# Kernel tuning notes

Hardware: AMD Instinct MI355X
Metric: run time of the kernel (lower is better)

The kernel has to match this reference:

```python
import jax, jax.numpy as jnp
import numpy as np

B, S, H, NH = 4, 2048, 1024, 16
D = H // NH  # head width = 64
SCALE = 1.0 / np.sqrt(np.float32(H))  # NOTE: module scales by rsqrt(hidden_size), not head_width
EPS = 1e-5


def setup_inputs() -> dict:
    key = jax.random.key(0)
    ks = jax.random.split(key, 12)
    def lin(k):
        kw, kb = jax.random.split(k)
        return (jax.random.normal(kw, (H, H), jnp.float32) * 0.02,
                jax.random.normal(kb, (H,), jnp.float32) * 0.02)
    Wq, bq = lin(ks[0]); Wk, bk = lin(ks[1]); Wv, bv = lin(ks[2]); Wm, bm = lin(ks[3])
    q = jax.random.normal(ks[4], (B, S, H), jnp.float32)
    k = jax.random.normal(ks[5], (B, S, H), jnp.float32)
    v = jax.random.normal(ks[6], (B, S, H), jnp.float32)
    # causal mask: True positions are masked with -inf (matches masked_fill semantics)
    mask = jnp.broadcast_to(jnp.triu(jnp.ones((S, S), bool), k=1), (B, S, S))
    gamma = jnp.ones((H,), jnp.float32)
    beta = jnp.zeros((H,), jnp.float32)
    return {"q": q, "k": k, "v": v, "mask": mask,
            "Wq": Wq, "bq": bq, "Wk": Wk, "bk": bk, "Wv": Wv, "bv": bv,
            "Wm": Wm, "bm": bm, "gamma": gamma, "beta": beta}


def layer_norm(x, gamma, beta):
    mu = jnp.mean(x, axis=-1, keepdims=True)
    var = jnp.mean(jnp.square(x - mu), axis=-1, keepdims=True)
    return (x - mu) * jax.lax.rsqrt(var + EPS) * gamma + beta


def reference(q, k, v, mask, Wq, bq, Wk, bk, Wv, bv, Wm, bm, gamma, beta):
    residual = q
    # projections, split into heads: [B, NH, S, D]
    qh = (q @ Wq.T + bq).reshape(B, S, NH, D).transpose(0, 2, 1, 3)
    kh = (k @ Wk.T + bk).reshape(B, S, NH, D).transpose(0, 2, 1, 3)
    vh = (v @ Wv.T + bv).reshape(B, S, NH, D).transpose(0, 2, 1, 3)
    scores = jnp.einsum('bhsd,bhtd->bhst', qh, kh) * SCALE
    scores = jnp.where(mask[:, None, :, :], -jnp.inf, scores)
    attn = jax.nn.softmax(scores, axis=-1)  # dropout is identity (p=0 / eval)
    ctx = jnp.einsum('bhst,bhtd->bhsd', attn, vh)
    ctx = ctx.transpose(0, 2, 1, 3).reshape(B, S, H)
    out = ctx @ Wm.T + bm
    out = layer_norm(out + residual, gamma, beta)
    return out, attn
```

## Files before the change

### kernel.cpp

```cpp
#include <hip/hip_runtime.h>
#include <hip/hip_bf16.h>

#define S_LEN   2048
#define NHEAD   16
#define HID     1024
#define HDIM    64
#define ATT_SCALE 0.03125f
#define LN_EPS  1e-5f
#define EXP_C1  0.04508422002778011f
#define EXP_C2  (-11.541560327111707f)

using bf16x8 = __attribute__((ext_vector_type(8))) short;
using f32x4  = __attribute__((ext_vector_type(4))) float;
using u16x8  = __attribute__((ext_vector_type(8))) unsigned short;
typedef unsigned short u16;

__device__ __forceinline__ u16 f2b(float f) {
  union { float f; unsigned u; } v; v.f = f;
  unsigned r = v.u + 0x7fffu + ((v.u >> 16) & 1u);
  return (u16)(r >> 16);
}

__device__ __forceinline__ float fexp2(float x) {
  return __builtin_amdgcn_exp2f(x);
}

__device__ __forceinline__ unsigned cvtpk(float a, float b) {
  unsigned r;
  asm("v_cvt_pk_bf16_f32 %0, %1, %2" : "=v"(r) : "v"(a), "v"(b));
  return r;
}

__device__ __forceinline__ f32x4 mfma16(bf16x8 a, bf16x8 b, f32x4 c) {
  return __builtin_amdgcn_mfma_f32_16x16x32_bf16(a, b, c, 0, 0, 0);
}

__device__ __forceinline__ void gld_lds16(const u16* g, void* l) {
  __builtin_amdgcn_global_load_lds(
      (const __attribute__((address_space(1))) void*)g,
      (__attribute__((address_space(3))) void*)l, 16, 0, 0);
}

__global__ void cvt_f32_bf16(const float* __restrict__ src, u16* __restrict__ dst, int n4) {
  int i = blockIdx.x * blockDim.x + threadIdx.x;
  int stride = gridDim.x * blockDim.x;
  for (; i < n4; i += stride) {
    float4 v = ((const float4*)src)[i];
    ushort4 o;
    o.x = f2b(v.x); o.y = f2b(v.y); o.z = f2b(v.z); o.w = f2b(v.w);
    ((ushort4*)dst)[i] = o;
  }
}

template<int EPI>
__global__ __launch_bounds__(256) void gemm_bt(
    const u16* __restrict__ A, const u16* __restrict__ W,
    const float* __restrict__ bias, u16* __restrict__ out_b,
    float* __restrict__ out_f, int M, int N, int K,
    float* __restrict__ fill, int fphase)
{
  __shared__ __align__(16) u16 As[128 * 64];
  __shared__ __align__(16) u16 Bs[128 * 64];
  const int t = threadIdx.x;

  if (blockIdx.y >= 64) {
    int u = (((int)blockIdx.y - 64) * 8 + (int)blockIdx.x) * 3 + fphase;
    if (u < 7680) {
      int bh = u & 63, tmp = u >> 6, qtb = tmp >> 3, rg = tmp & 7;
      int w4 = (15 - qtb) * 32;
      f32x4* base = (f32x4*)(fill + ((long)bh * 2048 + qtb * 128 + rg * 16) * 2048
                                  + (qtb + 1) * 128);
      f32x4 z = { 0.f, 0.f, 0.f, 0.f };
      for (int r = 0; r < 16; ++r) {
        f32x4* rp = base + (long)r * 512;
        for (int cc = t; cc < w4; cc += 256) rp[cc] = z;
      }
    }
    return;
  }

  const int m0 = blockIdx.y * 128, n0 = blockIdx.x * 128;
  const int w = t >> 6, lane = t & 63, g = lane >> 4, c = lane & 15;
  const int wr = w >> 1, wc = w & 1;

  f32x4 acc[4][4] = {};

  for (int k0 = 0; k0 < K; k0 += 64) {
    __syncthreads();
#pragma unroll
    for (int it = 0; it < 4; ++it) {
      int chunk = it * 256 + t;
      int row = chunk >> 3, cf = (chunk & 7) * 8;
      gld_lds16(&A[(long)(m0 + row) * K + k0 + cf], &As[(it * 256 + (t & ~63)) * 8]);
      gld_lds16(&W[(long)(n0 + row) * K + k0 + cf], &Bs[(it * 256 + (t & ~63)) * 8]);
    }
    __syncthreads();
#pragma unroll
    for (int kk = 0; kk < 2; ++kk) {
      bf16x8 am[4], bn[4];
#pragma unroll
      for (int m = 0; m < 4; ++m)
        am[m] = *(const bf16x8*)(&As[(wr * 64 + m * 16 + c) * 64 + kk * 32 + g * 8]);
#pragma unroll
      for (int n = 0; n < 4; ++n)
        bn[n] = *(const bf16x8*)(&Bs[(wc * 64 + n * 16 + c) * 64 + kk * 32 + g * 8]);
#pragma unroll
      for (int m = 0; m < 4; ++m)
#pragma unroll
        for (int n = 0; n < 4; ++n)
          acc[m][n] = mfma16(am[m], bn[n], acc[m][n]);
    }
  }

#pragma unroll
  for (int m = 0; m < 4; ++m)
#pragma unroll
    for (int n = 0; n < 4; ++n)
#pragma unroll
      for (int r = 0; r < 4; ++r) {
        int grow = m0 + wr * 64 + m * 16 + g * 4 + r;
        int gcol = n0 + wc * 64 + n * 16 + c;
        float v = acc[m][n][r];
        if (EPI == 0) {
          v += bias[gcol];
          int b = grow >> 11, s = grow & 2047;
          int h = gcol >> 6, d = gcol & 63;
          out_b[(((long)(b * 16 + h) * 2048 + s) << 6) + d] = f2b(v);
        } else {
          out_f[(long)grow * N + gcol] = v;
        }
      }
}

__global__ __launch_bounds__(256) void transpose_v(const u16* __restrict__ vh,
                                                   u16* __restrict__ vt) {
  __shared__ __align__(16) u16 tile[64 * 72];
  const int t = threadIdx.x;
  const u16* src = vh + ((long)blockIdx.y * 2048 + blockIdx.x * 64) * 64;
#pragma unroll
  for (int it = 0; it < 2; ++it) {
    int chunk = it * 256 + t;
    int s = chunk >> 3, d0 = (chunk & 7) * 8;
    *(int4*)(&tile[s * 72 + d0]) = *(const int4*)(&src[s * 64 + d0]);
  }
  __syncthreads();
  u16* dst = vt + (long)blockIdx.y * 64 * 2048 + blockIdx.x * 64;
#pragma unroll
  for (int it = 0; it < 2; ++it) {
    int chunk = it * 256 + t;
    int d = chunk >> 3, s0 = (chunk & 7) * 8;
    u16x8 v;
#pragma unroll
    for (int x = 0; x < 8; ++x) v[x] = tile[(s0 + x) * 72 + d];
    *(u16x8*)(&dst[(long)d * 2048 + s0]) = v;
  }
}

__global__ __launch_bounds__(512, 4) void attn_kernel(
    const u16* __restrict__ qh, const u16* __restrict__ kh,
    const u16* __restrict__ vt, u16* __restrict__ ctx,
    float* __restrict__ attn)
{
  __shared__ __align__(16) char lds[81920];
  const int t = threadIdx.x, w = t >> 6, lane = t & 63, g = lane >> 4, c = lane & 15;
  const int n = blockIdx.x;
  const int bh = (n & 7) * 8 + ((n >> 3) & 7);
  const int qtb = 15 - (n >> 6);
  const int q0 = qtb * 128;
  const int ktmax = qtb * 2 + 1;
  const long kvbase = (long)bh * 2048 * 64;

  bf16x8 qa[2];
  {
    const u16* qp = qh + kvbase + (long)(q0 + w * 16 + c) * 64 + g * 8;
    qa[0] = *(const bf16x8*)(qp);
    qa[1] = *(const bf16x8*)(qp + 32);
  }
  const int qpos = q0 + w * 16 + c;

  const int srow = t >> 3, sc8 = t & 7;
  const int ksoff = srow * 64 + ((sc8 ^ (srow & 7)) * 8);
  const u16* kbase = kh + kvbase;
  const u16* vbase = vt + (long)(bh * 64 + srow) * 2048 + ((sc8 ^ (srow & 7)) * 8);

  float lsum = 0.f;
  {
    gld_lds16(kbase + ksoff, lds + w * 1024);
    gld_lds16(kbase + 4096 + ksoff, lds + 8192 + w * 1024);
    for (int p = 0; p <= qtb; ++p) {
      const int kb = (p & 1) * 16384;
      if (p < qtb) {
        const int nb = ((p + 1) & 1) * 16384;
        gld_lds16(kbase + (long)(p + 1) * 8192 + ksoff, lds + nb + w * 1024);
        gld_lds16(kbase + (long)(p + 1) * 8192 + 4096 + ksoff, lds + nb + 8192 + w * 1024);
        asm volatile("s_waitcnt vmcnt(2)" ::: "memory");
      } else {
        asm volatile("s_waitcnt vmcnt(0)" ::: "memory");
      }
      __builtin_amdgcn_sched_barrier(0);
      __builtin_amdgcn_s_barrier();
      __builtin_amdgcn_sched_barrier(0);
      f32x4 sacc[8] = {};
      __builtin_amdgcn_s_setprio(1);
#pragma unroll
      for (int sub = 0; sub < 8; ++sub) {
        int row = sub * 16 + c;
#pragma unroll
        for (int kk = 0; kk < 2; ++kk) {
          bf16x8 av = *(const bf16x8*)(lds + kb + row * 128 + (((kk * 4 + g) ^ (c & 7)) << 4));
          sacc[sub] = mfma16(av, qa[kk], sacc[sub]);
        }
      }
      __builtin_amdgcn_s_setprio(0);
#pragma unroll
      for (int sub = 0; sub < 8; ++sub)
#pragma unroll
        for (int r = 0; r < 4; ++r) {
          int kpos = p * 128 + sub * 16 + g * 4 + r;
          float e = fexp2(fmaf(sacc[sub][r], EXP_C1, EXP_C2));
          lsum += (kpos > qpos) ? 0.f : e;
        }
      __builtin_amdgcn_sched_barrier(0);
      __builtin_amdgcn_s_barrier();
    }
  }
  lsum += __shfl_xor(lsum, 16, 64);
  lsum += __shfl_xor(lsum, 32, 64);
  const float ri = 1.f / lsum;

  char* const Ps = lds + 32768 + w * 2048;
  char* const Pf = lds + 49152 + w * 4096;
  f32x4 oacc[4] = {};
  gld_lds16(kbase + ksoff, lds + w * 1024);
  gld_lds16(vbase, lds + 16384 + w * 1024);
  for (int kt = 0; kt <= ktmax; ++kt) {
    const int kb = (kt & 1) * 8192;
    if (kt < ktmax) {
      const int nb = ((kt + 1) & 1) * 8192;
      gld_lds16(kbase + (long)(kt + 1) * 4096 + ksoff, lds + nb + w * 1024);
      gld_lds16(vbase + (kt + 1) * 64, lds + 16384 + nb + w * 1024);
      if (kt == 0) { asm volatile("s_waitcnt vmcnt(2)" ::: "memory"); }
      else         { asm volatile("s_waitcnt vmcnt(6)" ::: "memory"); }
    } else {
      asm volatile("s_waitcnt vmcnt(4)" ::: "memory");
    }
    __builtin_amdgcn_sched_barrier(0);
    __builtin_amdgcn_s_barrier();
    __builtin_amdgcn_sched_barrier(0);
    f32x4 sacc[4] = {};
    __builtin_amdgcn_s_setprio(1);
#pragma unroll
    for (int sub = 0; sub < 4; ++sub) {
      int row = sub * 16 + c;
#pragma unroll
      for (int kk = 0; kk < 2; ++kk) {
        bf16x8 av = *(const bf16x8*)(lds + kb + row * 128 + (((kk * 4 + g) ^ (c & 7)) << 4));
        sacc[sub] = mfma16(av, qa[kk], sacc[sub]);
      }
    }
    __builtin_amdgcn_s_setprio(0);
#pragma unroll
    for (int sub = 0; sub < 4; ++sub) {
      float p[4];
#pragma unroll
      for (int r = 0; r < 4; ++r) {
        int kpos = kt * 64 + sub * 16 + g * 4 + r;
        float e = fexp2(fmaf(sacc[sub][r], EXP_C1, EXP_C2)) * ri;
        p[r] = (kpos > qpos) ? 0.f : e;
      }
      f32x4 pv4 = { p[0], p[1], p[2], p[3] };
      int kgrp = sub * 4 + g;
      *(f32x4*)(Pf + c * 256 + ((kgrp ^ c) & 15) * 16) = pv4;
      uint2 pk = { cvtpk(p[0], p[1]), cvtpk(p[2], p[3]) };
      int chunk = sub * 2 + (g >> 1);
      *(uint2*)(Ps + c * 128 + ((chunk ^ (c & 7)) << 4) + (g & 1) * 8) = pk;
    }
    {
      float* arow0 = attn + ((long)bh * 2048 + q0 + w * 16) * 2048 + kt * 64;
#pragma unroll
      for (int j = 0; j < 4; ++j) {
        int row = j * 4 + g;
        f32x4 pv = *(const f32x4*)(Pf + row * 256 + ((c ^ row) & 15) * 16);
        *(f32x4*)(arow0 + (long)row * 2048 + c * 4) = pv;
      }
    }
    __builtin_amdgcn_s_setprio(1);
#pragma unroll
    for (int kk = 0; kk < 2; ++kk) {
      bf16x8 pa = *(const bf16x8*)(Ps + c * 128 + (((kk * 4 + g) ^ (c & 7)) << 4));
#pragma unroll
      for (int db = 0; db < 4; ++db) {
        bf16x8 vb = *(const bf16x8*)(lds + 16384 + kb + (db * 16 + c) * 128 + (((kk * 4 + g) ^ (c & 7)) << 4));
        oacc[db] = mfma16(pa, vb, oacc[db]);
      }
    }
    __builtin_amdgcn_s_setprio(0);
    __builtin_amdgcn_sched_barrier(0);
    __builtin_amdgcn_s_barrier();
  }

  {
    int b = bh >> 4, h = bh & 15;
#pragma unroll
    for (int db = 0; db < 4; ++db)
#pragma unroll
      for (int r = 0; r < 4; ++r) {
        int s = q0 + w * 16 + g * 4 + r;
        ctx[(long)(b * 2048 + s) * 1024 + h * 64 + db * 16 + c] = f2b(oacc[db][r]);
      }
  }
}

__global__ __launch_bounds__(256) void ln_kernel(
    const float* __restrict__ y, const float* __restrict__ bm,
    const float* __restrict__ resid, const float* __restrict__ gamma,
    const float* __restrict__ beta, float* __restrict__ out)
{
  __shared__ float red[8];
  const long row = blockIdx.x;
  const int t = threadIdx.x, w = t >> 6, lane = t & 63;
  const float4* yp = (const float4*)(y + row * 1024);
  const float4* rp = (const float4*)(resid + row * 1024);
  float4 x = yp[t], rv = rp[t], bv = ((const float4*)bm)[t];
  x.x += rv.x + bv.x; x.y += rv.y + bv.y; x.z += rv.z + bv.z; x.w += rv.w + bv.w;

  float s1 = x.x + x.y + x.z + x.w;
#pragma unroll
  for (int o = 32; o; o >>= 1) s1 += __shfl_xor(s1, o, 64);
  if (!lane) red[w] = s1;
  __syncthreads();
  float mean = (red[0] + red[1] + red[2] + red[3]) * (1.f / 1024.f);

  float dx = x.x - mean, dy = x.y - mean, dz = x.z - mean, dw = x.w - mean;
  float s2 = dx * dx + dy * dy + dz * dz + dw * dw;
#pragma unroll
  for (int o = 32; o; o >>= 1) s2 += __shfl_xor(s2, o, 64);
  if (!lane) red[4 + w] = s2;
  __syncthreads();
  float var = (red[4] + red[5] + red[6] + red[7]) * (1.f / 1024.f);
  float rs = rsqrtf(var + LN_EPS);

  float4 gv = ((const float4*)gamma)[t], be = ((const float4*)beta)[t];
  float4 o4;
  o4.x = dx * rs * gv.x + be.x;
  o4.y = dy * rs * gv.y + be.y;
  o4.z = dz * rs * gv.z + be.z;
  o4.w = dw * rs * gv.w + be.w;
  ((float4*)(out + row * 1024))[t] = o4;
}

extern "C" void kernel_launch(void* const* d_in, const int* in_sizes, int n_in,
                              void* d_out, int out_size, void* d_ws, size_t ws_size,
                              hipStream_t stream) {
  const float* q     = (const float*)d_in[0];
  const float* k     = (const float*)d_in[1];
  const float* v     = (const float*)d_in[2];
  const float* Wq    = (const float*)d_in[4];
  const float* bq    = (const float*)d_in[5];
  const float* Wk    = (const float*)d_in[6];
  const float* bk    = (const float*)d_in[7];
  const float* Wv    = (const float*)d_in[8];
  const float* bv    = (const float*)d_in[9];
  const float* Wm    = (const float*)d_in[10];
  const float* bm    = (const float*)d_in[11];
  const float* gamma = (const float*)d_in[12];
  const float* beta  = (const float*)d_in[13];

  float* out  = (float*)d_out;
  float* attn = out + 8388608;

  char* ws = (char*)d_ws;
  u16* qh   = (u16*)(ws);
  u16* kh   = (u16*)(ws + 16777216);
  u16* vt   = (u16*)(ws + 33554432);
  u16* ctx  = (u16*)(ws + 50331648);
  u16* Wqb  = (u16*)(ws + 67108864);
  u16* Wkb  = Wqb + 1048576;
  u16* Wvb  = Wkb + 1048576;
  u16* Wmb  = Wvb + 1048576;
  u16* xb   = (u16*)(ws + 75497472);
  u16* vh   = (u16*)(ws + 92274688);
  float* y  = (float*)(ws + 75497472);

  const int M = 8192, N = 1024, K = 1024;
  dim3 blk(256);
  dim3 ggrid(8, 64);
  dim3 ggridF(8, 64 + 320);

  cvt_f32_bf16<<<512, blk, 0, stream>>>(Wq, Wqb, 262144);
  cvt_f32_bf16<<<512, blk, 0, stream>>>(Wk, Wkb, 262144);
  cvt_f32_bf16<<<512, blk, 0, stream>>>(Wv, Wvb, 262144);
  cvt_f32_bf16<<<512, blk, 0, stream>>>(Wm, Wmb, 262144);

  cvt_f32_bf16<<<2048, blk, 0, stream>>>(q, xb, 2097152);
  gemm_bt<0><<<ggridF, blk, 0, stream>>>(xb, Wqb, bq, qh, nullptr, M, N, K, attn, 0);
  cvt_f32_bf16<<<2048, blk, 0, stream>>>(k, xb, 2097152);
  gemm_bt<0><<<ggridF, blk, 0, stream>>>(xb, Wkb, bk, kh, nullptr, M, N, K, attn, 1);
  cvt_f32_bf16<<<2048, blk, 0, stream>>>(v, xb, 2097152);
  gemm_bt<0><<<ggridF, blk, 0, stream>>>(xb, Wvb, bv, vh, nullptr, M, N, K, attn, 2);

  transpose_v<<<dim3(32, 64), blk, 0, stream>>>(vh, vt);

  attn_kernel<<<1024, 512, 0, stream>>>(qh, kh, vt, ctx, attn);

  gemm_bt<1><<<ggrid, blk, 0, stream>>>(ctx, Wmb, nullptr, nullptr, y, M, N, K, nullptr, 0);

  ln_kernel<<<8192, blk, 0, stream>>>(y, bm, q, gamma, beta, out);
}
```

Before: 508.1 us.

## Fuse input fp32-to-bf16 conversion into a single batched QKV projection GEMM

Merges the four weight conversions into one launch and replaces three separate convert-plus-GEMM pairs with a single QKV GEMM kernel. That kernel loads fp32 activations directly, packs them to bf16 in registers and stores them into LDS, with the causal-mask zero fill interleaved as extra blocks. This removes the intermediate bf16 activation buffer round-trip and several kernel launches. The cost is that A-tile loads now go through registers instead of async global-to-LDS copies and read twice the bytes. The vh workspace now aliases ctx.

```diff
diff --git a/kernel.cpp b/kernel.cpp
--- a/kernel.cpp
+++ b/kernel.cpp
@@ -12,7 +12,6 @@
 
 using bf16x8 = __attribute__((ext_vector_type(8))) short;
 using f32x4  = __attribute__((ext_vector_type(4))) float;
-using u16x8  = __attribute__((ext_vector_type(8))) unsigned short;
 typedef unsigned short u16;
 
 __device__ __forceinline__ u16 f2b(float f) {
@@ -41,58 +40,134 @@
       (__attribute__((address_space(3))) void*)l, 16, 0, 0);
 }
 
-__global__ void cvt_f32_bf16(const float* __restrict__ src, u16* __restrict__ dst, int n4) {
-  int i = blockIdx.x * blockDim.x + threadIdx.x;
-  int stride = gridDim.x * blockDim.x;
-  for (; i < n4; i += stride) {
-    float4 v = ((const float4*)src)[i];
+__global__ __launch_bounds__(256) void cvt_w4(
+    const float* __restrict__ s0, const float* __restrict__ s1,
+    const float* __restrict__ s2, const float* __restrict__ s3,
+    u16* __restrict__ d0, u16* __restrict__ d1,
+    u16* __restrict__ d2, u16* __restrict__ d3)
+{
+  int i = blockIdx.x * 256 + threadIdx.x;
+  int stride = gridDim.x * 256;
+  for (; i < 1048576; i += stride) {
+    int seg = i >> 18, off = i & 262143;
+    const float* s = seg == 0 ? s0 : seg == 1 ? s1 : seg == 2 ? s2 : s3;
+    u16*         d = seg == 0 ? d0 : seg == 1 ? d1 : seg == 2 ? d2 : d3;
+    float4 vv = ((const float4*)s)[off];
     ushort4 o;
-    o.x = f2b(v.x); o.y = f2b(v.y); o.z = f2b(v.z); o.w = f2b(v.w);
-    ((ushort4*)dst)[i] = o;
-  }
-}
-
-template<int EPI>
-__global__ __launch_bounds__(256) void gemm_bt(
+    o.x = f2b(vv.x); o.y = f2b(vv.y); o.z = f2b(vv.z); o.w = f2b(vv.w);
+    ((ushort4*)d)[off] = o;
+  }
+}
+
+__global__ __launch_bounds__(256) void qkv_gemm(
+    const float* __restrict__ qx, const float* __restrict__ kx,
+    const float* __restrict__ vx,
+    const u16* __restrict__ Wq, const u16* __restrict__ Wk,
+    const u16* __restrict__ Wv,
+    const float* __restrict__ bq, const float* __restrict__ bk,
+    const float* __restrict__ bv,
+    u16* __restrict__ qo, u16* __restrict__ ko, u16* __restrict__ vo,
+    float* __restrict__ fill)
+{
+  const int t = threadIdx.x;
+  const int yg = blockIdx.y / 6, yr = blockIdx.y % 6;
+
+  if (yr != 0) {
+    int u = (yg * 5 + (yr - 1)) * 8 + blockIdx.x;
+    int bh = u & 63, tmp = u >> 6, qtb = tmp >> 3, rg = tmp & 7;
+    int w4 = (15 - qtb) * 32;
+    f32x4* base = (f32x4*)(fill + ((long)bh * 2048 + qtb * 128 + rg * 16) * 2048
+                                + (qtb + 1) * 128);
+    f32x4 z = { 0.f, 0.f, 0.f, 0.f };
+    for (int r = 0; r < 16; ++r) {
+      f32x4* rp = base + (long)r * 512;
+      for (int cc = t; cc < w4; cc += 256) rp[cc] = z;
+    }
+    return;
+  }
+
+  const int op = yg >> 6;
+  const float* A32  = op == 0 ? qx : op == 1 ? kx : vx;
+  const u16*   W    = op == 0 ? Wq : op == 1 ? Wk : Wv;
+  const float* bias = op == 0 ? bq : op == 1 ? bk : bv;
+  u16*         out  = op == 0 ? qo : op == 1 ? ko : vo;
+
+  __shared__ __align__(16) u16 As[128 * 64];
+  __shared__ __align__(16) u16 Bs[128 * 64];
+  const int m0 = (yg & 63) * 128, n0 = blockIdx.x * 128;
+  const int w = t >> 6, lane = t & 63, g = lane >> 4, c = lane & 15;
+  const int wr = w >> 1, wc = w & 1;
+
+  f32x4 acc[4][4] = {};
+
+  for (int k0 = 0; k0 < 1024; k0 += 64) {
+    __syncthreads();
+#pragma unroll
+    for (int it = 0; it < 4; ++it) {
+      int chunk = it * 256 + t;
+      int row = chunk >> 3, cf = (chunk & 7) * 8;
+      const float* ap = &A32[(long)(m0 + row) * 1024 + k0 + cf];
+      float4 a0 = *(const float4*)(ap);
+      float4 a1 = *(const float4*)(ap + 4);
+      uint4 pk = { cvtpk(a0.x, a0.y), cvtpk(a0.z, a0.w),
+                   cvtpk(a1.x, a1.y), cvtpk(a1.z, a1.w) };
+      *(uint4*)(&As[chunk * 8]) = pk;
+      gld_lds16(&W[(long)(n0 + row) * 1024 + k0 + cf], &Bs[(it * 256 + (t & ~63)) * 8]);
+    }
+    __syncthreads();
+#pragma unroll
+    for (int kk = 0; kk < 2; ++kk) {
+      bf16x8 am[4], bn[4];
+#pragma unroll
+      for (int m = 0; m < 4; ++m)
+        am[m] = *(const bf16x8*)(&As[(wr * 64 + m * 16 + c) * 64 + kk * 32 + g * 8]);
+#pragma unroll
+      for (int n = 0; n < 4; ++n)
+        bn[n] = *(const bf16x8*)(&Bs[(wc * 64 + n * 16 + c) * 64 + kk * 32 + g * 8]);
+#pragma unroll
+      for (int m = 0; m < 4; ++m)
+#pragma unroll
+        for (int n = 0; n < 4; ++n)
+          acc[m][n] = mfma16(am[m], bn[n], acc[m][n]);
+    }
+  }
+
+#pragma unroll
+  for (int m = 0; m < 4; ++m)
+#pragma unroll
+    for (int n = 0; n < 4; ++n)
+#pragma unroll
+      for (int r = 0; r < 4; ++r) {
+        int grow = m0 + wr * 64 + m * 16 + g * 4 + r;
+        int gcol = n0 + wc * 64 + n * 16 + c;
+        float v = acc[m][n][r] + bias[gcol];
+        int b = grow >> 11, s = grow & 2047;
+        int h = gcol >> 6, d = gcol & 63;
+        out[(((long)(b * 16 + h) * 2048 + s) << 6) + d] = f2b(v);
+      }
+}
+
+__global__ __launch_bounds__(256) void gemm_out(
     const u16* __restrict__ A, const u16* __restrict__ W,
-    const float* __restrict__ bias, u16* __restrict__ out_b,
-    float* __restrict__ out_f, int M, int N, int K,
-    float* __restrict__ fill, int fphase)
+    float* __restrict__ out_f)
 {
   __shared__ __align__(16) u16 As[128 * 64];
   __shared__ __align__(16) u16 Bs[128 * 64];
   const int t = threadIdx.x;
-
-  if (blockIdx.y >= 64) {
-    int u = (((int)blockIdx.y - 64) * 8 + (int)blockIdx.x) * 3 + fphase;
-    if (u < 7680) {
-      int bh = u & 63, tmp = u >> 6, qtb = tmp >> 3, rg = tmp & 7;
-      int w4 = (15 - qtb) * 32;
-      f32x4* base = (f32x4*)(fill + ((long)bh * 2048 + qtb * 128 + rg * 16) * 2048
-                                  + (qtb + 1) * 128);
-      f32x4 z = { 0.f, 0.f, 0.f, 0.f };
-      for (int r = 0; r < 16; ++r) {
-        f32x4* rp = base + (long)r * 512;
-        for (int cc = t; cc < w4; cc += 256) rp[cc] = z;
-      }
-    }
-    return;
-  }
-
   const int m0 = blockIdx.y * 128, n0 = blockIdx.x * 128;
   const int w = t >> 6, lane = t & 63, g = lane >> 4, c = lane & 15;
   const int wr = w >> 1, wc = w & 1;
 
   f32x4 acc[4][4] = {};
 
-  for (int k0 = 0; k0 < K; k0 += 64) {
+  for (int k0 = 0; k0 < 1024; k0 += 64) {
     __syncthreads();
 #pragma unroll
     for (int it = 0; it < 4; ++it) {
       int chunk = it * 256 + t;
       int row = chunk >> 3, cf = (chunk & 7) * 8;
-      gld_lds16(&A[(long)(m0 + row) * K + k0 + cf], &As[(it * 256 + (t & ~63)) * 8]);
-      gld_lds16(&W[(long)(n0 + row) * K + k0 + cf], &Bs[(it * 256 + (t & ~63)) * 8]);
+      gld_lds16(&A[(long)(m0 + row) * 1024 + k0 + cf], &As[(it * 256 + (t & ~63)) * 8]);
+      gld_lds16(&W[(long)(n0 + row) * 1024 + k0 + cf], &Bs[(it * 256 + (t & ~63)) * 8]);
     }
     __syncthreads();
 #pragma unroll
@@ -120,15 +195,7 @@
       for (int r = 0; r < 4; ++r) {
         int grow = m0 + wr * 64 + m * 16 + g * 4 + r;
         int gcol = n0 + wc * 64 + n * 16 + c;
-        float v = acc[m][n][r];
-        if (EPI == 0) {
-          v += bias[gcol];
-          int b = grow >> 11, s = grow & 2047;
-          int h = gcol >> 6, d = gcol & 63;
-          out_b[(((long)(b * 16 + h) * 2048 + s) << 6) + d] = f2b(v);
-        } else {
-          out_f[(long)grow * N + gcol] = v;
-        }
+        out_f[(long)grow * 1024 + gcol] = acc[m][n][r];
       }
 }
 
@@ -149,10 +216,10 @@
   for (int it = 0; it < 2; ++it) {
     int chunk = it * 256 + t;
     int d = chunk >> 3, s0 = (chunk & 7) * 8;
-    u16x8 v;
+    __attribute__((ext_vector_type(8))) unsigned short v;
 #pragma unroll
     for (int x = 0; x < 8; ++x) v[x] = tile[(s0 + x) * 72 + d];
-    *(u16x8*)(&dst[(long)d * 2048 + s0]) = v;
+    *(decltype(v)*)(&dst[(long)d * 2048 + s0]) = v;
   }
 }
 
@@ -373,37 +440,26 @@
   u16* qh   = (u16*)(ws);
   u16* kh   = (u16*)(ws + 16777216);
   u16* vt   = (u16*)(ws + 33554432);
+  u16* vh   = (u16*)(ws + 50331648);
   u16* ctx  = (u16*)(ws + 50331648);
   u16* Wqb  = (u16*)(ws + 67108864);
   u16* Wkb  = Wqb + 1048576;
   u16* Wvb  = Wkb + 1048576;
   u16* Wmb  = Wvb + 1048576;
-  u16* xb   = (u16*)(ws + 75497472);
-  u16* vh   = (u16*)(ws + 92274688);
   float* y  = (float*)(ws + 75497472);
 
-  const int M = 8192, N = 1024, K = 1024;
   dim3 blk(256);
-  dim3 ggrid(8, 64);
-  dim3 ggridF(8, 64 + 320);
-
-  cvt_f32_bf16<<<512, blk, 0, stream>>>(Wq, Wqb, 262144);
-  cvt_f32_bf16<<<512, blk, 0, stream>>>(Wk, Wkb, 262144);
-  cvt_f32_bf16<<<512, blk, 0, stream>>>(Wv, Wvb, 262144);
-  cvt_f32_bf16<<<512, blk, 0, stream>>>(Wm, Wmb, 262144);
-
-  cvt_f32_bf16<<<2048, blk, 0, stream>>>(q, xb, 2097152);
-  gemm_bt<0><<<ggridF, blk, 0, stream>>>(xb, Wqb, bq, qh, nullptr, M, N, K, attn, 0);
-  cvt_f32_bf16<<<2048, blk, 0, stream>>>(k, xb, 2097152);
-  gemm_bt<0><<<ggridF, blk, 0, stream>>>(xb, Wkb, bk, kh, nullptr, M, N, K, attn, 1);
-  cvt_f32_bf16<<<2048, blk, 0, stream>>>(v, xb, 2097152);
-  gemm_bt<0><<<ggridF, blk, 0, stream>>>(xb, Wvb, bv, vh, nullptr, M, N, K, attn, 2);
+
+  cvt_w4<<<1024, blk, 0, stream>>>(Wq, Wk, Wv, Wm, Wqb, Wkb, Wvb, Wmb);
+
+  qkv_gemm<<<dim3(8, 1152), blk, 0, stream>>>(
+      q, k, v, Wqb, Wkb, Wvb, bq, bk, bv, qh, kh, vh, attn);
 
   transpose_v<<<dim3(32, 64), blk, 0, stream>>>(vh, vt);
 
   attn_kernel<<<1024, 512, 0, stream>>>(qh, kh, vt, ctx, attn);
 
-  gemm_bt<1><<<ggrid, blk, 0, stream>>>(ctx, Wmb, nullptr, nullptr, y, M, N, K, nullptr, 0);
+  gemm_out<<<dim3(8, 64), blk, 0, stream>>>(ctx, Wmb, y);
 
   ln_kernel<<<8192, blk, 0, stream>>>(y, bm, q, gamma, beta, out);
 }
```

Measured after the change: 583.5 us. 14.8% more time.
